# Optimization experiments

Hardware: AMD Instinct MI355X
Metric: run time of the kernel (lower is better)

## Reference

```python
import jax, jax.numpy as jnp
import numpy as np

N_NODES = 50000
N_EDGES = 600000
D_IN = 128
D_OUT = 128


def setup_inputs() -> dict:
    key = jax.random.key(0)
    k1, k2, k3, k4, k5, k6 = jax.random.split(key, 6)
    n_feats = jax.random.normal(k1, (N_NODES, D_IN), dtype=jnp.float32)
    e_weights = jax.random.uniform(k2, (N_EDGES, 1), dtype=jnp.float32)
    # Linear(in_dim*2, out_dim): W [out, 2*in], b [out]
    W = jax.random.normal(k3, (D_OUT, 2 * D_IN), dtype=jnp.float32) * 0.05
    b = jax.random.normal(k4, (D_OUT,), dtype=jnp.float32) * 0.05
    src = jax.random.randint(k5, (N_EDGES,), 0, N_NODES, dtype=jnp.int64)
    dst = jax.random.randint(k6, (N_EDGES,), 0, N_NODES, dtype=jnp.int64)
    return {"n_feats": n_feats, "e_weights": e_weights, "W": W, "b": b,
            "src": src, "dst": dst}


def reference(n_feats, e_weights, W, b, src, dst):
    N = n_feats.shape[0]
    # message: u_mul_e -> h[src] * ew   [E, D]
    msgs = n_feats[src] * e_weights
    # mean reduce over incoming edges (DGL fn.mean divides by in-degree)
    agg = jax.ops.segment_sum(msgs, dst, num_segments=N)  # [N, D]
    deg = jax.ops.segment_sum(jnp.ones((msgs.shape[0],), dtype=n_feats.dtype),
                              dst, num_segments=N)         # [N]
    h = agg / jnp.maximum(deg, 1.0)[:, None]               # zero-degree -> 0
    # concat aggregated + original, then linear
    z = jnp.concatenate([h, n_feats], axis=-1)             # [N, 2D]
    return z @ W.T + b
```

## Files before the change

kernel.cpp:

```cpp
#include <hip/hip_runtime.h>

#define N_NODES 50000
#define N_EDGES 600000
#define DIM 128
#define NF4N (N_NODES * DIM / 4)
#define WGN (256 * 128 / 8)
#define GEMM_TILES2 (((N_NODES + 63) / 64) * 2)
#define ZERO_BLOCKS ((N_NODES + 255) / 256)
#define BCAP 64

typedef __attribute__((ext_vector_type(8))) short short8;
typedef __attribute__((ext_vector_type(4))) float f32x4;

__device__ __forceinline__ unsigned bf16rne(float f) {
  unsigned x = __float_as_uint(f);
  x += 0x7fffu + ((x >> 16) & 1u);
  return x >> 16;
}

__device__ __forceinline__ uint2 pack4(float4 v) {
  uint2 o;
  o.x = bf16rne(v.x) | (bf16rne(v.y) << 16);
  o.y = bf16rne(v.z) | (bf16rne(v.w) << 16);
  return o;
}

__device__ __forceinline__ void fma8(float* a, uint4 v, float w) {
  a[0] += __uint_as_float(v.x << 16) * w;
  a[1] += __uint_as_float(v.x & 0xffff0000u) * w;
  a[2] += __uint_as_float(v.y << 16) * w;
  a[3] += __uint_as_float(v.y & 0xffff0000u) * w;
  a[4] += __uint_as_float(v.z << 16) * w;
  a[5] += __uint_as_float(v.z & 0xffff0000u) * w;
  a[6] += __uint_as_float(v.w << 16) * w;
  a[7] += __uint_as_float(v.w & 0xffff0000u) * w;
}

__global__ __launch_bounds__(256) void k_zero(int* __restrict__ deg) {
  int i = blockIdx.x * 256 + threadIdx.x;
  if (i < N_NODES) deg[i] = 0;
}

__global__ __launch_bounds__(256) void k_histscat_cvt(
    const int* __restrict__ dst, const int* __restrict__ src,
    const float* __restrict__ ew, int* __restrict__ deg,
    unsigned* __restrict__ srcw,
    const float4* __restrict__ nf4, uint2* __restrict__ nf16d,
    const float* __restrict__ Wf, uint4* __restrict__ wtS) {
  int gid = blockIdx.x * 256 + threadIdx.x;

  int d = 0, rk = 0;
  unsigned rec = 0;
  bool isE = (gid < N_EDGES);
  if (isE) {
    d = dst[gid];
    rk = atomicAdd(&deg[d], 1);
    unsigned wq = (unsigned)rintf(ew[gid] * 65535.0f);
    rec = (unsigned)src[gid] | (wq << 16);
  }

  if (gid < WGN) {
    int j = gid >> 4, cb = gid & 15;
    int jr = (j < 128) ? j : (j - 128);
    int c0 = ((j < 128) ? 0 : 128) + cb * 8;
    const float4* s = reinterpret_cast<const float4*>(Wf + (size_t)jr * 256 + c0);
    uint2 lo = pack4(s[0]);
    uint2 hi = pack4(s[1]);
    int jb = j >> 4, l16 = j & 15, ks = cb >> 2, lg = cb & 3;
    wtS[((jb * 4 + ks) * 64) + lg * 16 + l16] = make_uint4(lo.x, lo.y, hi.x, hi.y);
  }
  if (gid < NF4N) nf16d[gid] = pack4(nf4[gid]);

  if (isE) srcw[d * BCAP + rk] = rec;
}

__global__ __launch_bounds__(256) void k_gemm(
    const char* __restrict__ nf16, const uint4* __restrict__ wtS,
    const float* __restrict__ bias,
    unsigned short* __restrict__ y1, unsigned short* __restrict__ y2) {
  __shared__ char As[16384];
  const int tileN = blockIdx.x >> 1;
  const int jsel = blockIdx.x & 1;
  const int node0 = tileN * 64;
  const int tid = threadIdx.x;

#pragma unroll
  for (int i = 0; i < 4; ++i) {
    int G = tid + i * 256;
    int r = G >> 4, g = G & 15;
    int node = node0 + r;
    if (node > N_NODES - 1) node = N_NODES - 1;
    uint4 v = *reinterpret_cast<const uint4*>(nf16 + (size_t)node * 256 + g * 16);
    *reinterpret_cast<uint4*>(As + r * 256 + ((g ^ (r & 7)) * 16)) = v;
  }
  __syncthreads();

  const int lane = tid & 63;
  const int wv = tid >> 6;
  const int l16 = lane & 15, lg = lane >> 4;

  f32x4 acc[4][2] = {};
#pragma unroll
  for (int ks = 0; ks < 4; ++ks) {
    short8 anf[4], awt[2];
#pragma unroll
    for (int m = 0; m < 4; ++m) {
      int r = m * 16 + l16;
      int g = ks * 4 + lg;
      anf[m] = *reinterpret_cast<const short8*>(As + r * 256 + ((g ^ (r & 7)) * 16));
    }
#pragma unroll
    for (int n = 0; n < 2; ++n) {
      int jb = jsel * 8 + wv * 2 + n;
      const uint4* fp = wtS + (jb * 4 + ks) * 64 + lane;
      uint4 v = *fp;
      awt[n] = *reinterpret_cast<const short8*>(&v);
    }
#pragma unroll
    for (int m = 0; m < 4; ++m)
#pragma unroll
      for (int n = 0; n < 2; ++n)
        acc[m][n] = __builtin_amdgcn_mfma_f32_16x16x32_bf16(awt[n], anf[m], acc[m][n], 0, 0, 0);
  }

  unsigned short* yb = jsel ? y2 : y1;
#pragma unroll
  for (int n = 0; n < 2; ++n) {
    int jb = (wv * 2 + n) * 16 + lg * 4;
    float4 bv = make_float4(0.f, 0.f, 0.f, 0.f);
    if (jsel) bv = *reinterpret_cast<const float4*>(bias + jb);
#pragma unroll
    for (int m = 0; m < 4; ++m) {
      int node = node0 + m * 16 + l16;
      if (node >= N_NODES) continue;
      uint2 st;
      st.x = bf16rne(acc[m][n][0] + bv.x) | (bf16rne(acc[m][n][1] + bv.y) << 16);
      st.y = bf16rne(acc[m][n][2] + bv.z) | (bf16rne(acc[m][n][3] + bv.w) << 16);
      *reinterpret_cast<uint2*>(yb + (size_t)node * 128 + jb) = st;
    }
  }
}

__global__ __launch_bounds__(256) void k_gather(
    const uint4* __restrict__ y1q,
    const uint4* __restrict__ y2q,
    const int* __restrict__ deg, const unsigned* __restrict__ srcw,
    float4* __restrict__ out4) {
  int node = blockIdx.x * 4 + (threadIdx.x >> 6);
  int lane = threadIdx.x & 63;
  int g = lane >> 3;
  int c = lane & 7;
  int dg = deg[node];
  const unsigned* bucket = srcw + (size_t)node * BCAP;

  float a[16];
#pragma unroll
  for (int k = 0; k < 16; ++k) a[k] = 0.f;

  for (int j = g; j < dg; j += 8) {
    unsigned q = bucket[j];
    float w = (float)(q >> 16) * (1.0f / 65535.0f);
    const uint4* rp = y1q + (size_t)(q & 0xffffu) * 16 + c * 2;
    uint4 v0 = rp[0];
    uint4 v1 = rp[1];
    fma8(a, v0, w);
    fma8(a + 8, v1, w);
  }
#pragma unroll
  for (int k = 0; k < 16; ++k) {
    a[k] += __shfl_xor(a[k], 8);
    a[k] += __shfl_xor(a[k], 16);
    a[k] += __shfl_xor(a[k], 32);
  }
  if (g == 0) {
    float inv = 1.0f / (float)max(dg, 1);
    uint4 u0 = y2q[(size_t)node * 16 + c * 2];
    uint4 u1 = y2q[(size_t)node * 16 + c * 2 + 1];
    float4 o0, o1, o2, o3;
    o0.x = a[0] * inv + __uint_as_float(u0.x << 16);
    o0.y = a[1] * inv + __uint_as_float(u0.x & 0xffff0000u);
    o0.z = a[2] * inv + __uint_as_float(u0.y << 16);
    o0.w = a[3] * inv + __uint_as_float(u0.y & 0xffff0000u);
    o1.x = a[4] * inv + __uint_as_float(u0.z << 16);
    o1.y = a[5] * inv + __uint_as_float(u0.z & 0xffff0000u);
    o1.z = a[6] * inv + __uint_as_float(u0.w << 16);
    o1.w = a[7] * inv + __uint_as_float(u0.w & 0xffff0000u);
    o2.x = a[8] * inv + __uint_as_float(u1.x << 16);
    o2.y = a[9] * inv + __uint_as_float(u1.x & 0xffff0000u);
    o2.z = a[10] * inv + __uint_as_float(u1.y << 16);
    o2.w = a[11] * inv + __uint_as_float(u1.y & 0xffff0000u);
    o3.x = a[12] * inv + __uint_as_float(u1.z << 16);
    o3.y = a[13] * inv + __uint_as_float(u1.z & 0xffff0000u);
    o3.z = a[14] * inv + __uint_as_float(u1.w << 16);
    o3.w = a[15] * inv + __uint_as_float(u1.w & 0xffff0000u);
    float4* op = out4 + (size_t)node * 32 + c * 4;
    op[0] = o0; op[1] = o1; op[2] = o2; op[3] = o3;
  }
}

extern "C" void kernel_launch(void* const* d_in, const int* in_sizes, int n_in,
                              void* d_out, int out_size, void* d_ws, size_t ws_size,
                              hipStream_t stream) {
  const float* nf  = (const float*)d_in[0];
  const float* ew  = (const float*)d_in[1];
  const float* W   = (const float*)d_in[2];
  const float* b   = (const float*)d_in[3];
  const int*   src = (const int*)d_in[4];
  const int*   dst = (const int*)d_in[5];
  float* out = (float*)d_out;

  char* ws = (char*)d_ws;
  char* nf16 = ws;
  char* wtS  = nf16 + (size_t)N_NODES * DIM * 2;
  char* y1   = wtS + (size_t)WGN * 16;
  char* y2   = y1 + (size_t)N_NODES * DIM * 2;
  int*  deg  = (int*)(y2 + (size_t)N_NODES * DIM * 2);
  unsigned* srcw = (unsigned*)(deg + N_NODES + 60);

  k_zero<<<ZERO_BLOCKS, 256, 0, stream>>>(deg);
  k_histscat_cvt<<<NF4N / 256, 256, 0, stream>>>(
      dst, src, ew, deg, srcw, (const float4*)nf, (uint2*)nf16, W, (uint4*)wtS);
  k_gemm<<<GEMM_TILES2, 256, 0, stream>>>(
      nf16, (const uint4*)wtS, b, (unsigned short*)y1, (unsigned short*)y2);
  k_gather<<<N_NODES / 4, 256, 0, stream>>>(
      (const uint4*)y1, (const uint4*)y2, deg, srcw, (float4*)out);
}
```

Before: 90.10 us.

## Fold degree zeroing into init and co-schedule edge histogram with GEMM

```diff
diff --git a/kernel.cpp b/kernel.cpp
--- a/kernel.cpp
+++ b/kernel.cpp
@@ -5,8 +5,9 @@
 #define DIM 128
 #define NF4N (N_NODES * DIM / 4)
 #define WGN (256 * 128 / 8)
-#define GEMM_TILES2 (((N_NODES + 63) / 64) * 2)
-#define ZERO_BLOCKS ((N_NODES + 255) / 256)
+#define GEMM_PAIRS ((N_NODES + 63) / 64)
+#define HIST_SLICES ((N_EDGES + 255) / 256)
+#define K2_BLOCKS (GEMM_PAIRS * 5)
 #define BCAP 64
 
 typedef __attribute__((ext_vector_type(8))) short short8;
@@ -36,29 +37,12 @@
   a[7] += __uint_as_float(v.w & 0xffff0000u) * w;
 }
 
-__global__ __launch_bounds__(256) void k_zero(int* __restrict__ deg) {
-  int i = blockIdx.x * 256 + threadIdx.x;
-  if (i < N_NODES) deg[i] = 0;
-}
-
-__global__ __launch_bounds__(256) void k_histscat_cvt(
-    const int* __restrict__ dst, const int* __restrict__ src,
-    const float* __restrict__ ew, int* __restrict__ deg,
-    unsigned* __restrict__ srcw,
+__global__ __launch_bounds__(256) void k_init(
+    int* __restrict__ deg,
     const float4* __restrict__ nf4, uint2* __restrict__ nf16d,
     const float* __restrict__ Wf, uint4* __restrict__ wtS) {
   int gid = blockIdx.x * 256 + threadIdx.x;
-
-  int d = 0, rk = 0;
-  unsigned rec = 0;
-  bool isE = (gid < N_EDGES);
-  if (isE) {
-    d = dst[gid];
-    rk = atomicAdd(&deg[d], 1);
-    unsigned wq = (unsigned)rintf(ew[gid] * 65535.0f);
-    rec = (unsigned)src[gid] | (wq << 16);
-  }
-
+  if (gid < N_NODES) deg[gid] = 0;
   if (gid < WGN) {
     int j = gid >> 4, cb = gid & 15;
     int jr = (j < 128) ? j : (j - 128);
@@ -70,18 +54,35 @@
     wtS[((jb * 4 + ks) * 64) + lg * 16 + l16] = make_uint4(lo.x, lo.y, hi.x, hi.y);
   }
   if (gid < NF4N) nf16d[gid] = pack4(nf4[gid]);
-
-  if (isE) srcw[d * BCAP + rk] = rec;
-}
-
-__global__ __launch_bounds__(256) void k_gemm(
+}
+
+__global__ __launch_bounds__(256) void k_gemm_histscat(
+    const int* __restrict__ dst, const int* __restrict__ src,
+    const float* __restrict__ ew, int* __restrict__ deg,
+    unsigned* __restrict__ srcw,
     const char* __restrict__ nf16, const uint4* __restrict__ wtS,
     const float* __restrict__ bias,
     unsigned short* __restrict__ y1, unsigned short* __restrict__ y2) {
   __shared__ char As[16384];
-  const int tileN = blockIdx.x >> 1;
-  const int jsel = blockIdx.x & 1;
-  const int node0 = tileN * 64;
+  const int grp = blockIdx.x / 5;
+  const int sub = blockIdx.x % 5;
+
+  if (sub >= 2) {
+    int hb = grp * 3 + (sub - 2);
+    if (hb < HIST_SLICES) {
+      int e = hb * 256 + threadIdx.x;
+      if (e < N_EDGES) {
+        int d = dst[e];
+        int rk = atomicAdd(&deg[d], 1);
+        unsigned wq = (unsigned)rintf(ew[e] * 65535.0f);
+        srcw[d * BCAP + rk] = (unsigned)src[e] | (wq << 16);
+      }
+    }
+    return;
+  }
+
+  const int node0 = grp * 64;
+  const int jsel = sub;
   const int tid = threadIdx.x;
 
 #pragma unroll
@@ -217,11 +218,11 @@
   int*  deg  = (int*)(y2 + (size_t)N_NODES * DIM * 2);
   unsigned* srcw = (unsigned*)(deg + N_NODES + 60);
 
-  k_zero<<<ZERO_BLOCKS, 256, 0, stream>>>(deg);
-  k_histscat_cvt<<<NF4N / 256, 256, 0, stream>>>(
-      dst, src, ew, deg, srcw, (const float4*)nf, (uint2*)nf16, W, (uint4*)wtS);
-  k_gemm<<<GEMM_TILES2, 256, 0, stream>>>(
-      nf16, (const uint4*)wtS, b, (unsigned short*)y1, (unsigned short*)y2);
+  k_init<<<NF4N / 256, 256, 0, stream>>>(
+      deg, (const float4*)nf, (uint2*)nf16, W, (uint4*)wtS);
+  k_gemm_histscat<<<K2_BLOCKS, 256, 0, stream>>>(
+      dst, src, ew, deg, srcw, nf16, (const uint4*)wtS, b,
+      (unsigned short*)y1, (unsigned short*)y2);
   k_gather<<<N_NODES / 4, 256, 0, stream>>>(
       (const uint4*)y1, (const uint4*)y2, deg, srcw, (float4*)out);
 }
```

After: 78.68 us. -12.7%, faster.
